# Kernel tuning notes

Hardware: AMD Instinct MI355X
Metric: run time of the kernel (lower is better)

The kernel has to match this reference:

```python
import jax, jax.numpy as jnp
import numpy as np

K = 9
DILATION = 2


def pairwise_distance(x):
    # x: (B, N, C) -> (B, N, N) squared Euclidean distances
    x_inner = -2.0 * jnp.einsum('bnc,bmc->bnm', x, x)
    x_square = jnp.sum(x * x, axis=-1, keepdims=True)  # (B, N, 1)
    return x_square + x_inner + jnp.swapaxes(x_square, 1, 2)


def setup_inputs() -> dict:
    key = jax.random.key(0)
    x = jax.random.normal(key, (4, 64, 4096, 1), dtype=jnp.float32)
    return {"x": x}


def reference(x):
    # x: (B, C, N, 1) -> (B, N, C)
    xt = jnp.swapaxes(x, 1, 2)[..., 0]
    B, N, C = xt.shape
    k_eff = K * DILATION
    neg_dist = -pairwise_distance(xt)  # (B, N, N)
    _, nn_idx = jax.lax.top_k(neg_dist, k_eff)  # (B, N, k_eff)
    center_idx = jnp.broadcast_to(jnp.arange(N)[None, :, None], (B, N, k_eff))
    edge_index = jnp.stack((nn_idx, center_idx), axis=0)  # (2, B, N, k_eff)
    # dilated selection: every DILATION-th neighbor -> (2, B, N, K)
    return edge_index[:, :, :, ::DILATION]
```

## Files before the change

kernel.cpp:

```cpp
#include <hip/hip_runtime.h>


#pragma clang fp contract(off)

#define BB    4
#define CDIM  64
#define NPTS  4096
#define KSEL  17
#define KOUT  9

__global__ __launch_bounds__(256) void knn_sq(const float* __restrict__ x,
                                              float* __restrict__ sq) {
#pragma clang fp contract(off)
    int g = blockIdx.x * 256 + threadIdx.x;
    int b = g >> 12;
    int m = g & (NPTS - 1);
    const float* xb = x + (size_t)b * CDIM * NPTS + m;

    float a[CDIM];
    #pragma unroll
    for (int c = 0; c < CDIM; ++c) {
        float v = xb[c * NPTS];
        a[c] = v * v;
    }
    float s16[16];
    #pragma unroll
    for (int i = 0; i < 16; ++i)
        s16[i] = (a[i] + a[i + 16]) + (a[i + 32] + a[i + 48]);
    float t8[8];
    #pragma unroll
    for (int i = 0; i < 8; ++i) t8[i] = s16[i] + s16[i + 8];
    float t4[4];
    #pragma unroll
    for (int i = 0; i < 4; ++i) t4[i] = t8[i] + t8[i + 4];
    float u0 = t4[0] + t4[2];
    float u1 = t4[1] + t4[3];
    sq[g] = u0 + u1;
}

__global__ __launch_bounds__(256) void knn_main(const float* __restrict__ x,
                                                const float* __restrict__ sq,
                                                int* __restrict__ out) {
#pragma clang fp contract(off)
    const int bx = blockIdx.x;
    const int b  = bx >> 12;
    const int n  = bx & (NPTS - 1);
    const int t  = threadIdx.x;

    __shared__ float qs[CDIM];
    __shared__ float redD[4];
    __shared__ int   redI[4];
    __shared__ int   sel[KSEL];

    const float* xb = x + (size_t)b * CDIM * NPTS;
    if (t < CDIM) qs[t] = xb[t * NPTS + n];
    __syncthreads();

    const float* sqb = sq + (b << 12);
    const float  sqn = sqb[n];

    float d[16];
    {
        const float q0 = qs[0];
        const float* xr = xb + t;
        #pragma unroll
        for (int i = 0; i < 16; ++i) d[i] = q0 * xr[256 * i];
    }
    for (int c = 1; c < CDIM; ++c) {
        const float qc = qs[c];
        const float* xr = xb + c * NPTS + t;
        #pragma unroll
        for (int i = 0; i < 16; ++i) {
            float p = qc * xr[256 * i];
            d[i] = d[i] + p;
        }
    }

    float key[16];
    #pragma unroll
    for (int i = 0; i < 16; ++i) {
        float inner = -2.0f * d[i];
        float t1    = sqn + inner;
        key[i]      = t1 + sqb[t + 256 * i];
    }

    unsigned mask = 0;
    for (int r = 0; r < KSEL; ++r) {
        float best = 3.0e38f;
        int   bi   = 0x7fffffff;
        #pragma unroll
        for (int i = 0; i < 16; ++i) {
            float v = key[i];
            int   m = t + 256 * i;
            bool alive = !((mask >> i) & 1u);
            if (alive && (v < best || (v == best && m < bi))) { best = v; bi = m; }
        }
        #pragma unroll
        for (int off = 32; off >= 1; off >>= 1) {
            float od = __shfl_down(best, off);
            int   oi = __shfl_down(bi, off);
            if (od < best || (od == best && oi < bi)) { best = od; bi = oi; }
        }
        int w = t >> 6;
        if ((t & 63) == 0) { redD[w] = best; redI[w] = bi; }
        __syncthreads();
        float gb = redD[0];
        int   gi = redI[0];
        #pragma unroll
        for (int w2 = 1; w2 < 4; ++w2) {
            float od = redD[w2];
            int   oi = redI[w2];
            if (od < gb || (od == gb && oi < gi)) { gb = od; gi = oi; }
        }
        if (t == 0) sel[r] = gi;
        if ((gi & 255) == t) mask |= 1u << (gi >> 8);
        __syncthreads();
    }

    if (t < KOUT) {
        size_t base = (size_t)bx * KOUT;
        out[base + t] = sel[2 * t];
        out[(size_t)BB * NPTS * KOUT + base + t] = n;
    }
}

extern "C" void kernel_launch(void* const* d_in, const int* in_sizes, int n_in,
                              void* d_out, int out_size, void* d_ws, size_t ws_size,
                              hipStream_t stream) {
    const float* x   = (const float*)d_in[0];
    float*       sqv = (float*)d_ws;
    int*         out = (int*)d_out;

    hipLaunchKernelGGL(knn_sq,   dim3((BB * NPTS) / 256), dim3(256), 0, stream, x, sqv);
    hipLaunchKernelGGL(knn_main, dim3(BB * NPTS),         dim3(256), 0, stream, x, sqv, out);
}
```

Measured before the change: 631.8 us.

## Process four query points per block with contiguous float4 candidate loads

Each block now handles four query points, so every candidate-point load is reused across four dot products instead of one. Each thread owns 16 contiguous candidates, loaded as float4. The top-k selection keeps a cached per-thread minimum that is recomputed only by the thread whose candidate was chosen, and double-buffered reduction slots cut one barrier per round. Register pressure rises with 64 accumulators per thread, and the launch bound now requests four blocks per SM.

Result: slower. 1.200 ms (+89.9%).

```diff
diff --git a/kernel.cpp b/kernel.cpp
--- a/kernel.cpp
+++ b/kernel.cpp
@@ -8,6 +8,7 @@
 #define NPTS  4096
 #define KSEL  17
 #define KOUT  9
+#define QB    4
 
 __global__ __launch_bounds__(256) void knn_sq(const float* __restrict__ x,
                                               float* __restrict__ sq) {
@@ -38,89 +39,127 @@
     sq[g] = u0 + u1;
 }
 
-__global__ __launch_bounds__(256) void knn_main(const float* __restrict__ x,
-                                                const float* __restrict__ sq,
-                                                int* __restrict__ out) {
+__global__ __launch_bounds__(256, 4) void knn_main(const float* __restrict__ x,
+                                                   const float* __restrict__ sq,
+                                                   int* __restrict__ out) {
 #pragma clang fp contract(off)
-    const int bx = blockIdx.x;
-    const int b  = bx >> 12;
-    const int n  = bx & (NPTS - 1);
-    const int t  = threadIdx.x;
+    const int blk = blockIdx.x;
+    const int b   = blk >> 10;
+    const int n0  = (blk & 1023) * QB;
+    const int t   = threadIdx.x;
 
-    __shared__ float qs[CDIM];
-    __shared__ float redD[4];
-    __shared__ int   redI[4];
-    __shared__ int   sel[KSEL];
+    __shared__ float qs[QB][CDIM];
+    __shared__ float redD[2][4];
+    __shared__ int   redI[2][4];
 
     const float* xb = x + (size_t)b * CDIM * NPTS;
-    if (t < CDIM) qs[t] = xb[t * NPTS + n];
+
+    {
+        int q = t >> 6, c = t & 63;
+        qs[q][c] = xb[c * NPTS + n0 + q];
+    }
     __syncthreads();
 
     const float* sqb = sq + (b << 12);
-    const float  sqn = sqb[n];
 
-    float d[16];
+    float acc[QB][16];
     {
-        const float q0 = qs[0];
-        const float* xr = xb + t;
+        const float4* xr = (const float4*)(xb + 16 * t);
+        float4 v0 = xr[0], v1 = xr[1], v2 = xr[2], v3 = xr[3];
+        float xv[16] = {v0.x, v0.y, v0.z, v0.w, v1.x, v1.y, v1.z, v1.w,
+                        v2.x, v2.y, v2.z, v2.w, v3.x, v3.y, v3.z, v3.w};
         #pragma unroll
-        for (int i = 0; i < 16; ++i) d[i] = q0 * xr[256 * i];
+        for (int q = 0; q < QB; ++q) {
+            float qc = qs[q][0];
+            #pragma unroll
+            for (int j = 0; j < 16; ++j) acc[q][j] = qc * xv[j];
+        }
     }
+    #pragma unroll 2
     for (int c = 1; c < CDIM; ++c) {
-        const float qc = qs[c];
-        const float* xr = xb + c * NPTS + t;
+        const float4* xr = (const float4*)(xb + c * NPTS + 16 * t);
+        float4 v0 = xr[0], v1 = xr[1], v2 = xr[2], v3 = xr[3];
+        float xv[16] = {v0.x, v0.y, v0.z, v0.w, v1.x, v1.y, v1.z, v1.w,
+                        v2.x, v2.y, v2.z, v2.w, v3.x, v3.y, v3.z, v3.w};
         #pragma unroll
-        for (int i = 0; i < 16; ++i) {
-            float p = qc * xr[256 * i];
-            d[i] = d[i] + p;
+        for (int q = 0; q < QB; ++q) {
+            float qc = qs[q][c];
+            #pragma unroll
+            for (int j = 0; j < 16; ++j) {
+                float p = qc * xv[j];
+                acc[q][j] = acc[q][j] + p;
+            }
         }
     }
 
-    float key[16];
-    #pragma unroll
-    for (int i = 0; i < 16; ++i) {
-        float inner = -2.0f * d[i];
-        float t1    = sqn + inner;
-        key[i]      = t1 + sqb[t + 256 * i];
+    float sqm[16];
+    {
+        const float4* sr = (const float4*)(sqb + 16 * t);
+        float4 s0 = sr[0], s1 = sr[1], s2 = sr[2], s3 = sr[3];
+        sqm[0]=s0.x; sqm[1]=s0.y; sqm[2]=s0.z; sqm[3]=s0.w;
+        sqm[4]=s1.x; sqm[5]=s1.y; sqm[6]=s1.z; sqm[7]=s1.w;
+        sqm[8]=s2.x; sqm[9]=s2.y; sqm[10]=s2.z; sqm[11]=s2.w;
+        sqm[12]=s3.x; sqm[13]=s3.y; sqm[14]=s3.z; sqm[15]=s3.w;
     }
 
-    unsigned mask = 0;
-    for (int r = 0; r < KSEL; ++r) {
-        float best = 3.0e38f;
-        int   bi   = 0x7fffffff;
+    #pragma unroll
+    for (int q = 0; q < QB; ++q) {
+        const float sqn = sqb[n0 + q];
         #pragma unroll
-        for (int i = 0; i < 16; ++i) {
-            float v = key[i];
-            int   m = t + 256 * i;
-            bool alive = !((mask >> i) & 1u);
-            if (alive && (v < best || (v == best && m < bi))) { best = v; bi = m; }
+        for (int j = 0; j < 16; ++j) {
+            float inner = -2.0f * acc[q][j];
+            float t1    = sqn + inner;
+            acc[q][j]   = t1 + sqm[j];
         }
+
+        unsigned mask = 0;
+        float cm = 3.0e38f;
+        int   ci = 0x7fffffff;
         #pragma unroll
-        for (int off = 32; off >= 1; off >>= 1) {
-            float od = __shfl_down(best, off);
-            int   oi = __shfl_down(bi, off);
-            if (od < best || (od == best && oi < bi)) { best = od; bi = oi; }
+        for (int j = 0; j < 16; ++j) {
+            float v = acc[q][j];
+            if (v < cm) { cm = v; ci = 16 * t + j; }
         }
-        int w = t >> 6;
-        if ((t & 63) == 0) { redD[w] = best; redI[w] = bi; }
-        __syncthreads();
-        float gb = redD[0];
-        int   gi = redI[0];
-        #pragma unroll
-        for (int w2 = 1; w2 < 4; ++w2) {
-            float od = redD[w2];
-            int   oi = redI[w2];
-            if (od < gb || (od == gb && oi < gi)) { gb = od; gi = oi; }
+
+        int myOut = 0;
+        for (int r = 0; r < KSEL; ++r) {
+            const int p = (q + r) & 1;
+            float bd = cm;
+            int   bi = ci;
+            #pragma unroll
+            for (int off = 32; off >= 1; off >>= 1) {
+                float od = __shfl_down(bd, off);
+                int   oi = __shfl_down(bi, off);
+                if (od < bd || (od == bd && oi < bi)) { bd = od; bi = oi; }
+            }
+            if ((t & 63) == 0) { redD[p][t >> 6] = bd; redI[p][t >> 6] = bi; }
+            __syncthreads();
+            float gb = redD[p][0];
+            int   gi = redI[p][0];
+            #pragma unroll
+            for (int w = 1; w < 4; ++w) {
+                float od = redD[p][w];
+                int   oi = redI[p][w];
+                if (od < gb || (od == gb && oi < gi)) { gb = od; gi = oi; }
+            }
+            if (t < KOUT && r == 2 * t) myOut = gi;
+            if ((gi >> 4) == t) {
+                mask |= 1u << (gi & 15);
+                cm = 3.0e38f; ci = 0x7fffffff;
+                #pragma unroll
+                for (int j = 0; j < 16; ++j) {
+                    float v = acc[q][j];
+                    if (!((mask >> j) & 1u) && v < cm) { cm = v; ci = 16 * t + j; }
+                }
+            }
         }
-        if (t == 0) sel[r] = gi;
-        if ((gi & 255) == t) mask |= 1u << (gi >> 8);
-        __syncthreads();
-    }
 
-    if (t < KOUT) {
-        size_t base = (size_t)bx * KOUT;
-        out[base + t] = sel[2 * t];
-        out[(size_t)BB * NPTS * KOUT + base + t] = n;
+        if (t < KOUT) {
+            int    nq   = n0 + q;
+            size_t base = (size_t)((b << 12) + nq) * KOUT;
+            out[base + t] = myOut;
+            out[(size_t)BB * NPTS * KOUT + base + t] = nq;
+        }
     }
 }
 
@@ -132,5 +171,5 @@
     int*         out = (int*)d_out;
 
     hipLaunchKernelGGL(knn_sq,   dim3((BB * NPTS) / 256), dim3(256), 0, stream, x, sqv);
-    hipLaunchKernelGGL(knn_main, dim3(BB * NPTS),         dim3(256), 0, stream, x, sqv, out);
+    hipLaunchKernelGGL(knn_main, dim3((BB * NPTS) / QB),  dim3(256), 0, stream, x, sqv, out);
 }
```

## Process four queries per block with per-wave top-k lists and merge

Applied to the files above, without the earlier changes.

Each block now handles four query points with 1024 threads. Each thread holds four candidates per query, loaded as float4, so every load of x is reused across four queries. The top-k selection is restructured: each wave independently extracts its 17 smallest candidates via xor shuffles with a cached per-thread minimum, and a final per-query wave merges the 16 wave lists. This removes the two block-wide barriers per selection round and cuts global traffic, at the cost of more registers and shared memory per block.

Measured after the change: 1.044 ms. +65.3%, slower.

```diff
diff --git a/kernel.cpp b/kernel.cpp
--- a/kernel.cpp
+++ b/kernel.cpp
@@ -8,6 +8,10 @@
 #define NPTS  4096
 #define KSEL  17
 #define KOUT  9
+#define QB    4
+#define MPT   4
+#define NT    1024
+#define NW    (NT / 64)
 
 __global__ __launch_bounds__(256) void knn_sq(const float* __restrict__ x,
                                               float* __restrict__ sq) {
@@ -38,89 +42,152 @@
     sq[g] = u0 + u1;
 }
 
-__global__ __launch_bounds__(256) void knn_main(const float* __restrict__ x,
-                                                const float* __restrict__ sq,
-                                                int* __restrict__ out) {
+__global__ __launch_bounds__(NT) void knn_main(const float* __restrict__ x,
+                                               const float* __restrict__ sq,
+                                               int* __restrict__ out) {
 #pragma clang fp contract(off)
-    const int bx = blockIdx.x;
-    const int b  = bx >> 12;
-    const int n  = bx & (NPTS - 1);
-    const int t  = threadIdx.x;
-
-    __shared__ float qs[CDIM];
-    __shared__ float redD[4];
-    __shared__ int   redI[4];
-    __shared__ int   sel[KSEL];
-
-    const float* xb = x + (size_t)b * CDIM * NPTS;
-    if (t < CDIM) qs[t] = xb[t * NPTS + n];
+    const int blk  = blockIdx.x;
+    const int b    = blk >> 10;
+    const int n0   = (blk & 1023) * QB;
+    const int t    = threadIdx.x;
+    const int lane = t & 63;
+    const int wv   = t >> 6;
+
+    __shared__ float4 qT[CDIM];
+    __shared__ float  lK[QB][NW][KSEL];
+    __shared__ int    lI[QB][NW][KSEL];
+
+    const float* xb  = x + (size_t)b * CDIM * NPTS;
+    const float* sqb = sq + (b << 12);
+    const float* xp  = xb + MPT * t;
+
+    if (t < CDIM * QB) {
+        int c = t >> 2, qi = t & 3;
+        ((float*)&qT[c])[qi] = xb[(size_t)c * NPTS + n0 + qi];
+    }
     __syncthreads();
 
-    const float* sqb = sq + (b << 12);
-    const float  sqn = sqb[n];
-
-    float d[16];
+    float acc0[MPT], acc1[MPT], acc2[MPT], acc3[MPT];
     {
-        const float q0 = qs[0];
-        const float* xr = xb + t;
+        float4 xv = *(const float4*)(xp);
+        float4 qq = qT[0];
+        const float xvj[4] = {xv.x, xv.y, xv.z, xv.w};
         #pragma unroll
-        for (int i = 0; i < 16; ++i) d[i] = q0 * xr[256 * i];
-    }
+        for (int j = 0; j < 4; ++j) {
+            acc0[j] = qq.x * xvj[j];
+            acc1[j] = qq.y * xvj[j];
+            acc2[j] = qq.z * xvj[j];
+            acc3[j] = qq.w * xvj[j];
+        }
+    }
+    #pragma unroll 4
     for (int c = 1; c < CDIM; ++c) {
-        const float qc = qs[c];
-        const float* xr = xb + c * NPTS + t;
+        float4 xv = *(const float4*)(xp + (size_t)c * NPTS);
+        float4 qq = qT[c];
+        const float xvj[4] = {xv.x, xv.y, xv.z, xv.w};
         #pragma unroll
-        for (int i = 0; i < 16; ++i) {
-            float p = qc * xr[256 * i];
-            d[i] = d[i] + p;
-        }
-    }
-
-    float key[16];
-    #pragma unroll
-    for (int i = 0; i < 16; ++i) {
-        float inner = -2.0f * d[i];
-        float t1    = sqn + inner;
-        key[i]      = t1 + sqb[t + 256 * i];
-    }
-
-    unsigned mask = 0;
+        for (int j = 0; j < 4; ++j) {
+            float p0 = qq.x * xvj[j];
+            acc0[j] = acc0[j] + p0;
+            float p1 = qq.y * xvj[j];
+            acc1[j] = acc1[j] + p1;
+            float p2 = qq.z * xvj[j];
+            acc2[j] = acc2[j] + p2;
+            float p3 = qq.w * xvj[j];
+            acc3[j] = acc3[j] + p3;
+        }
+    }
+
+    float sqm[4];
+    {
+        float4 s = *(const float4*)(sqb + MPT * t);
+        sqm[0] = s.x; sqm[1] = s.y; sqm[2] = s.z; sqm[3] = s.w;
+    }
+    const float sqn0 = sqb[n0], sqn1 = sqb[n0 + 1];
+    const float sqn2 = sqb[n0 + 2], sqn3 = sqb[n0 + 3];
+    #pragma unroll
+    for (int j = 0; j < 4; ++j) {
+        { float in0 = -2.0f * acc0[j]; float t1 = sqn0 + in0; acc0[j] = t1 + sqm[j]; }
+        { float in1 = -2.0f * acc1[j]; float t1 = sqn1 + in1; acc1[j] = t1 + sqm[j]; }
+        { float in2 = -2.0f * acc2[j]; float t1 = sqn2 + in2; acc2[j] = t1 + sqm[j]; }
+        { float in3 = -2.0f * acc3[j]; float t1 = sqn3 + in3; acc3[j] = t1 + sqm[j]; }
+    }
+
+    unsigned msk0 = 0, msk1 = 0, msk2 = 0, msk3 = 0;
+    float cm0, cm1, cm2, cm3;
+    int   ci0, ci1, ci2, ci3;
+
+#define INIT_CM(CM, CI, ACC)                                                   \
+    { CM = 3.0e38f; CI = 0x7fffffff;                                           \
+      _Pragma("unroll")                                                        \
+      for (int j = 0; j < 4; ++j) {                                            \
+          float v = ACC[j];                                                    \
+          if (v < CM) { CM = v; CI = MPT * t + j; }                            \
+      } }
+    INIT_CM(cm0, ci0, acc0)
+    INIT_CM(cm1, ci1, acc1)
+    INIT_CM(cm2, ci2, acc2)
+    INIT_CM(cm3, ci3, acc3)
+
+#define RESCAN(CM, CI, MSK, ACC)                                               \
+    { CM = 3.0e38f; CI = 0x7fffffff;                                           \
+      _Pragma("unroll")                                                        \
+      for (int j = 0; j < 4; ++j) {                                            \
+          float v = ACC[j];                                                    \
+          if (!((MSK >> j) & 1u) && v < CM) { CM = v; CI = MPT * t + j; }      \
+      } }
+
     for (int r = 0; r < KSEL; ++r) {
-        float best = 3.0e38f;
-        int   bi   = 0x7fffffff;
+        float g0 = cm0, g1 = cm1, g2 = cm2, g3 = cm3;
+        int   i0 = ci0, i1 = ci1, i2 = ci2, i3 = ci3;
         #pragma unroll
-        for (int i = 0; i < 16; ++i) {
-            float v = key[i];
-            int   m = t + 256 * i;
-            bool alive = !((mask >> i) & 1u);
-            if (alive && (v < best || (v == best && m < bi))) { best = v; bi = m; }
-        }
-        #pragma unroll
-        for (int off = 32; off >= 1; off >>= 1) {
-            float od = __shfl_down(best, off);
-            int   oi = __shfl_down(bi, off);
-            if (od < best || (od == best && oi < bi)) { best = od; bi = oi; }
-        }
-        int w = t >> 6;
-        if ((t & 63) == 0) { redD[w] = best; redI[w] = bi; }
-        __syncthreads();
-        float gb = redD[0];
-        int   gi = redI[0];
-        #pragma unroll
-        for (int w2 = 1; w2 < 4; ++w2) {
-            float od = redD[w2];
-            int   oi = redI[w2];
-            if (od < gb || (od == gb && oi < gi)) { gb = od; gi = oi; }
-        }
-        if (t == 0) sel[r] = gi;
-        if ((gi & 255) == t) mask |= 1u << (gi >> 8);
-        __syncthreads();
-    }
-
-    if (t < KOUT) {
-        size_t base = (size_t)bx * KOUT;
-        out[base + t] = sel[2 * t];
-        out[(size_t)BB * NPTS * KOUT + base + t] = n;
+        for (int s = 1; s <= 32; s <<= 1) {
+            float o0 = __shfl_xor(g0, s); int j0 = __shfl_xor(i0, s);
+            if (o0 < g0 || (o0 == g0 && j0 < i0)) { g0 = o0; i0 = j0; }
+            float o1 = __shfl_xor(g1, s); int j1 = __shfl_xor(i1, s);
+            if (o1 < g1 || (o1 == g1 && j1 < i1)) { g1 = o1; i1 = j1; }
+            float o2 = __shfl_xor(g2, s); int j2 = __shfl_xor(i2, s);
+            if (o2 < g2 || (o2 == g2 && j2 < i2)) { g2 = o2; i2 = j2; }
+            float o3 = __shfl_xor(g3, s); int j3 = __shfl_xor(i3, s);
+            if (o3 < g3 || (o3 == g3 && j3 < i3)) { g3 = o3; i3 = j3; }
+        }
+        if (lane == 0) {
+            lK[0][wv][r] = g0; lI[0][wv][r] = i0;
+            lK[1][wv][r] = g1; lI[1][wv][r] = i1;
+            lK[2][wv][r] = g2; lI[2][wv][r] = i2;
+            lK[3][wv][r] = g3; lI[3][wv][r] = i3;
+        }
+        if (i0 == ci0) { msk0 |= 1u << (i0 & 3); RESCAN(cm0, ci0, msk0, acc0) }
+        if (i1 == ci1) { msk1 |= 1u << (i1 & 3); RESCAN(cm1, ci1, msk1, acc1) }
+        if (i2 == ci2) { msk2 |= 1u << (i2 & 3); RESCAN(cm2, ci2, msk2, acc2) }
+        if (i3 == ci3) { msk3 |= 1u << (i3 & 3); RESCAN(cm3, ci3, msk3, acc3) }
+    }
+
+    __syncthreads();
+
+    if (wv < QB) {
+        const int q = wv;
+        float hk; int hi; int hp = 0;
+        if (lane < NW) { hk = lK[q][lane][0]; hi = lI[q][lane][0]; }
+        else           { hk = 3.0e38f;        hi = 0x7fffffff;     }
+        const int    nq   = n0 + q;
+        const size_t base = (size_t)((b << 12) + nq) * KOUT;
+        for (int r = 0; r < KSEL; ++r) {
+            float gk = hk; int gi = hi;
+            #pragma unroll
+            for (int s = 1; s <= 8; s <<= 1) {
+                float ok = __shfl_xor(gk, s); int oi = __shfl_xor(gi, s);
+                if (ok < gk || (ok == gk && oi < gi)) { gk = ok; gi = oi; }
+            }
+            if ((r & 1) == 0 && lane == 0) out[base + (r >> 1)] = gi;
+            if (lane < NW && gi == hi) {
+                ++hp;
+                if (hp < KSEL) { hk = lK[q][lane][hp]; hi = lI[q][lane][hp]; }
+                else           { hk = 3.0e38f;         hi = 0x7fffffff;      }
+            }
+        }
+        if (lane < KOUT)
+            out[(size_t)BB * NPTS * KOUT + base + lane] = nq;
     }
 }
 
@@ -132,5 +199,5 @@
     int*         out = (int*)d_out;
 
     hipLaunchKernelGGL(knn_sq,   dim3((BB * NPTS) / 256), dim3(256), 0, stream, x, sqv);
-    hipLaunchKernelGGL(knn_main, dim3(BB * NPTS),         dim3(256), 0, stream, x, sqv, out);
+    hipLaunchKernelGGL(knn_main, dim3((BB * NPTS) / QB),  dim3(NT),  0, stream, x, sqv, out);
 }
```
